# Performance work log

Measured on AMD Instinct MI355X. Metric: run time of the kernel, lower is better.

The kernel has to match this reference:

```python
import jax, jax.numpy as jnp
import numpy as np

N = 100000        # nodes
E = 1600000       # edges (avg degree 16)
F_IN = 512        # num_features
H1, D1 = 8, 8     # layer-1 heads x per-head dim (concat -> 64)
C = 16            # num_classes (layer-2: 1 head, dim C)
NEG_SLOPE = 0.2


def setup_inputs() -> dict:
    key = jax.random.key(0)
    ks = jax.random.split(key, 8)
    x = jax.random.normal(ks[0], (N, F_IN), dtype=jnp.float32)
    edge_index = jax.random.randint(ks[1], (2, E), 0, N, dtype=jnp.int64)
    W1 = jax.random.normal(ks[2], (F_IN, H1 * D1), dtype=jnp.float32) / np.float32(np.sqrt(F_IN))
    a1_src = jax.random.normal(ks[3], (H1, D1), dtype=jnp.float32) * 0.1
    a1_dst = jax.random.normal(ks[4], (H1, D1), dtype=jnp.float32) * 0.1
    W2 = jax.random.normal(ks[5], (H1 * D1, C), dtype=jnp.float32) / np.float32(np.sqrt(H1 * D1))
    a2_src = jax.random.normal(ks[6], (1, C), dtype=jnp.float32) * 0.1
    a2_dst = jax.random.normal(ks[7], (1, C), dtype=jnp.float32) * 0.1
    return {"x": x, "edge_index": edge_index, "W1": W1, "a1_src": a1_src,
            "a1_dst": a1_dst, "W2": W2, "a2_src": a2_src, "a2_dst": a2_dst}


def gat_layer(x, src, dst, W, a_s, a_d, heads, out_dim):
    """Multi-head GAT conv: gather -> per-edge leaky-relu score -> segment
    softmax over destination -> scatter-aggregate. Returns [N, heads, out_dim]."""
    n = x.shape[0]
    h = (x @ W).reshape(n, heads, out_dim)            # [N, H, D]
    es = jnp.einsum('nhd,hd->nh', h, a_s)             # source attention term
    ed = jnp.einsum('nhd,hd->nh', h, a_d)             # dest attention term
    e = jax.nn.leaky_relu(es[src] + ed[dst], NEG_SLOPE)   # [E, H]
    m = jax.ops.segment_max(e, dst, num_segments=n)       # stable softmax max
    ex = jnp.exp(e - m[dst])
    s = jax.ops.segment_sum(ex, dst, num_segments=n)
    alpha = ex / s[dst]                               # [E, H]
    out = jax.ops.segment_sum(h[src] * alpha[..., None], dst, num_segments=n)
    return out                                        # [N, H, D]


def reference(x, edge_index, W1, a1_src, a1_dst, W2, a2_src, a2_dst):
    n = x.shape[0]
    loop = jnp.arange(n, dtype=edge_index.dtype)
    src = jnp.concatenate([edge_index[0], loop])      # add self-loops
    dst = jnp.concatenate([edge_index[1], loop])
    # eval mode: dropout(p=0.6, training=False) is identity
    h1 = gat_layer(x, src, dst, W1, a1_src, a1_dst, H1, D1).reshape(n, H1 * D1)
    h1 = jax.nn.elu(h1)
    h2 = gat_layer(h1, src, dst, W2, a2_src, a2_dst, 1, C).reshape(n, C)
    return jax.nn.log_softmax(h2, axis=1)
```

## Files before the change

### kernel.cpp

```cpp
#include <hip/hip_runtime.h>
#include <hip/hip_bf16.h>

#define F_IN 512
#define H1 8
#define D1 8
#define F_MID 64
#define C 16
#define NEG_SLOPE 0.2f
#define BIN_CHUNK 4096
#define NB_MAX 1024
#define BUCKET_SHIFT 7
#define BUCKET_STRIDE 3072

typedef __attribute__((ext_vector_type(8))) short bf16x8;
typedef __attribute__((ext_vector_type(4))) float f32x4;

static __device__ __forceinline__ unsigned short f2bf(float f) {
    __hip_bfloat16 h = __float2bfloat16(f);
    return *(unsigned short*)&h;
}

__global__ __launch_bounds__(256) void k_bin(const int* __restrict__ src,
                                             const int* __restrict__ dst,
                                             int* __restrict__ gcur,
                                             int2* __restrict__ bucketed,
                                             int n_edges, int nb) {
    __shared__ int cnt[NB_MAX];
    __shared__ int base[NB_MAX];
    const int t = threadIdx.x;
    const int eb = blockIdx.x * BIN_CHUNK;
    for (int b = t; b < nb; b += 256) cnt[b] = 0;
    __syncthreads();
#pragma unroll
    for (int i = 0; i < BIN_CHUNK / 256; ++i) {
        int e = eb + i * 256 + t;
        if (e < n_edges) atomicAdd(&cnt[dst[e] >> BUCKET_SHIFT], 1);
    }
    __syncthreads();
    for (int b = t; b < nb; b += 256) {
        int c = cnt[b];
        base[b] = c > 0 ? atomicAdd(&gcur[b], c) : 0;
        cnt[b] = 0;
    }
    __syncthreads();
#pragma unroll
    for (int i = 0; i < BIN_CHUNK / 256; ++i) {
        int e = eb + i * 256 + t;
        if (e < n_edges) {
            int d = dst[e];
            int b = d >> BUCKET_SHIFT;
            int local = atomicAdd(&cnt[b], 1);
            bucketed[(size_t)b * BUCKET_STRIDE + base[b] + local] = make_int2(src[e], d);
        }
    }
}

__global__ __launch_bounds__(1024) void k_bscan(const int* __restrict__ gcur,
                                                int* __restrict__ bucket_base,
                                                int* __restrict__ row_start_last,
                                                int nb, int n_edges_total) {
    __shared__ int sh[1024];
    const int t = threadIdx.x;
    const int v = (t < nb) ? gcur[t] : 0;
    sh[t] = v;
    __syncthreads();
#pragma unroll
    for (int d = 1; d < 1024; d <<= 1) {
        int u = (t >= d) ? sh[t - d] : 0;
        __syncthreads();
        sh[t] += u;
        __syncthreads();
    }
    if (t < nb) bucket_base[t] = sh[t] - v;
    if (t == 0) *row_start_last = n_edges_total;
}

__global__ __launch_bounds__(256) void k_place(const int* __restrict__ gcur,
                                               const int* __restrict__ bucket_base,
                                               const int2* __restrict__ bucketed,
                                               int* __restrict__ row_start,
                                               int* __restrict__ sorted_src, int n_nodes) {
    __shared__ int2 stage[BUCKET_STRIDE];
    __shared__ int cnt[1 << BUCKET_SHIFT];
    __shared__ int cur[1 << BUCKET_SHIFT];
    const int t = threadIdx.x;
    const int b = blockIdx.x;
    if (t < (1 << BUCKET_SHIFT)) cnt[t] = 0;
    __syncthreads();
    const int total = gcur[b];
    const int2* bp = bucketed + (size_t)b * BUCKET_STRIDE;
    for (int i = t; i < total; i += 256) {
        int2 e = bp[i];
        stage[i] = e;
        atomicAdd(&cnt[e.y & ((1 << BUCKET_SHIFT) - 1)], 1);
    }
    __syncthreads();
    if (t < (1 << BUCKET_SHIFT)) cur[t] = cnt[t];
    __syncthreads();
#pragma unroll
    for (int d = 1; d < (1 << BUCKET_SHIFT); d <<= 1) {
        int u = 0;
        if (t < (1 << BUCKET_SHIFT) && t >= d) u = cur[t - d];
        __syncthreads();
        if (t < (1 << BUCKET_SHIFT)) cur[t] += u;
        __syncthreads();
    }
    const int base0 = bucket_base[b];
    if (t < (1 << BUCKET_SHIFT)) {
        int node = (b << BUCKET_SHIFT) + t;
        int excl = cur[t] - cnt[t];
        if (node < n_nodes) row_start[node] = base0 + excl;
        cur[t] = excl;
    }
    __syncthreads();
    for (int i = t; i < total; i += 256) {
        int2 e = stage[i];
        int p = atomicAdd(&cur[e.y & ((1 << BUCKET_SHIFT) - 1)], 1);
        sorted_src[base0 + p] = e.x;
    }
}

__global__ __launch_bounds__(256) void k_w1t(const float* __restrict__ W1,
                                             __hip_bfloat16* __restrict__ w1t) {
    int idx = blockIdx.x * 256 + threadIdx.x;
    int k = idx >> 6, n = idx & 63;
    w1t[n * F_IN + k] = __float2bfloat16(W1[idx]);
}

__global__ __launch_bounds__(256) void k_gemm1(const float* __restrict__ x,
                                               const __hip_bfloat16* __restrict__ w1t,
                                               const float* __restrict__ a1s,
                                               const float* __restrict__ a1d,
                                               __hip_bfloat16* __restrict__ h1b,
                                               float* __restrict__ es1,
                                               float* __restrict__ ed1, int n_nodes) {
    __shared__ unsigned short Xs[64][72];
    __shared__ unsigned short Ws[64][72];
    __shared__ float sas[64], sad[64];
    const int t = threadIdx.x;
    if (t < 64) sas[t] = a1s[t];
    else if (t < 128) sad[t - 64] = a1d[t - 64];

    const int wv = t >> 6, l = t & 63;
    const int q = l >> 4, m16 = l & 15;
    const int rowbase = blockIdx.x * 64;

    const int sr = t >> 2, sf = t & 3;
    int gx = rowbase + sr;
    gx = gx < n_nodes ? gx : n_nodes - 1;
    const float* xrow = x + (size_t)gx * F_IN;
    const __hip_bfloat16* wrow = w1t + (size_t)sr * F_IN;

    f32x4 acc[4];
#pragma unroll
    for (int i = 0; i < 4; ++i) acc[i] = (f32x4){0.f, 0.f, 0.f, 0.f};

    for (int kt = 0; kt < F_IN; kt += 64) {
#pragma unroll
        for (int j = 0; j < 4; ++j) {
            float4 v = *(const float4*)(xrow + kt + sf * 16 + j * 4);
            ushort4 b;
            b.x = f2bf(v.x); b.y = f2bf(v.y); b.z = f2bf(v.z); b.w = f2bf(v.w);
            *(ushort4*)&Xs[sr][sf * 16 + j * 4] = b;
        }
#pragma unroll
        for (int j = 0; j < 2; ++j) {
            *(int4*)&Ws[sr][sf * 16 + j * 8] =
                *(const int4*)(wrow + kt + sf * 16 + j * 8);
        }
        __syncthreads();
#pragma unroll
        for (int kk = 0; kk < 2; ++kk) {
            bf16x8 bfrag = *(const bf16x8*)&Xs[wv * 16 + m16][kk * 32 + q * 8];
#pragma unroll
            for (int tn = 0; tn < 4; ++tn) {
                bf16x8 afrag = *(const bf16x8*)&Ws[tn * 16 + m16][kk * 32 + q * 8];
                acc[tn] = __builtin_amdgcn_mfma_f32_16x16x32_bf16(afrag, bfrag, acc[tn], 0, 0, 0);
            }
        }
        __syncthreads();
    }

    const int node = rowbase + wv * 16 + m16;
    const bool ok = node < n_nodes;
#pragma unroll
    for (int tn = 0; tn < 4; ++tn) {
        const f32x4 a = acc[tn];
        const int nw0 = tn * 16 + q * 4;
        float vs = a.x * sas[nw0] + a.y * sas[nw0 + 1] + a.z * sas[nw0 + 2] + a.w * sas[nw0 + 3];
        float vd = a.x * sad[nw0] + a.y * sad[nw0 + 1] + a.z * sad[nw0 + 2] + a.w * sad[nw0 + 3];
        vs += __shfl_xor(vs, 16, 64);
        vd += __shfl_xor(vd, 16, 64);
        if (ok) {
            ushort4 b;
            b.x = f2bf(a.x); b.y = f2bf(a.y); b.z = f2bf(a.z); b.w = f2bf(a.w);
            *(ushort4*)(h1b + (size_t)node * F_MID + nw0) = b;
            if ((q & 1) == 0) {
                const int head = 2 * tn + (q >> 1);
                es1[node * H1 + head] = vs;
                ed1[node * H1 + head] = vd;
            }
        }
    }
}

__global__ __launch_bounds__(256) void k_gather1(const int* __restrict__ row_start,
                                                 const int* __restrict__ sorted_src,
                                                 const __hip_bfloat16* __restrict__ h1b,
                                                 const float* __restrict__ es1,
                                                 const float* __restrict__ ed1,
                                                 float* __restrict__ h1, int n_nodes) {
    const int n = blockIdx.x * 4 + (threadIdx.x >> 6);
    if (n >= n_nodes) return;
    const int lane = threadIdx.x & 63;
    const int h = lane >> 3;
    const float edh = ed1[n * H1 + h];
    const int beg = row_start[n], end = row_start[n + 1];
    float acc = 0.f, den = 0.f;
    for (int base = beg; base < end; base += 64) {
        const int m = min(64, end - base);
        const int li = lane < m ? lane : (m - 1);
        const int myS = sorted_src[base + li];
        int j = 0;
        for (; j + 4 <= m; j += 4) {
            const int s0 = __shfl(myS, j, 64), s1 = __shfl(myS, j + 1, 64);
            const int s2 = __shfl(myS, j + 2, 64), s3 = __shfl(myS, j + 3, 64);
            float e0 = es1[s0 * H1 + h], e1 = es1[s1 * H1 + h];
            float e2 = es1[s2 * H1 + h], e3 = es1[s3 * H1 + h];
            const float f0 = __bfloat162float(h1b[(size_t)s0 * F_MID + lane]);
            const float f1 = __bfloat162float(h1b[(size_t)s1 * F_MID + lane]);
            const float f2 = __bfloat162float(h1b[(size_t)s2 * F_MID + lane]);
            const float f3 = __bfloat162float(h1b[(size_t)s3 * F_MID + lane]);
            e0 += edh; e1 += edh; e2 += edh; e3 += edh;
            e0 = e0 > 0.f ? e0 : NEG_SLOPE * e0;
            e1 = e1 > 0.f ? e1 : NEG_SLOPE * e1;
            e2 = e2 > 0.f ? e2 : NEG_SLOPE * e2;
            e3 = e3 > 0.f ? e3 : NEG_SLOPE * e3;
            const float w0 = __expf(e0), w1 = __expf(e1), w2 = __expf(e2), w3 = __expf(e3);
            acc += w0 * f0 + w1 * f1 + w2 * f2 + w3 * f3;
            den += (w0 + w1) + (w2 + w3);
        }
        for (; j < m; ++j) {
            const int s = __shfl(myS, j, 64);
            float ev = es1[s * H1 + h] + edh;
            ev = ev > 0.f ? ev : NEG_SLOPE * ev;
            const float w = __expf(ev);
            acc += w * __bfloat162float(h1b[(size_t)s * F_MID + lane]);
            den += w;
        }
    }
    float evs = es1[n * H1 + h] + edh;
    evs = evs > 0.f ? evs : NEG_SLOPE * evs;
    const float ws = __expf(evs);
    acc += ws * __bfloat162float(h1b[(size_t)n * F_MID + lane]);
    den += ws;
    float v = acc / den;
    v = v > 0.f ? v : expm1f(v);
    h1[(size_t)n * F_MID + lane] = v;
}

__global__ void k_gemm2(const float* __restrict__ h1, const float* __restrict__ W2,
                        const float* __restrict__ a2s, const float* __restrict__ a2d,
                        __hip_bfloat16* __restrict__ h2b, float* __restrict__ es2,
                        float* __restrict__ ed2, int n_nodes) {
    __shared__ float w2s[F_MID * C];
    __shared__ float h1s[16][F_MID + 1];
    const int t = threadIdx.x;
    const int nb = blockIdx.x * 16;
    for (int i = t; i < F_MID * C; i += 256) w2s[i] = W2[i];
    for (int i = t; i < 16 * F_MID; i += 256) {
        int r = i >> 6, k = i & 63;
        int n = nb + r;
        h1s[r][k] = h1[(size_t)(n < n_nodes ? n : n_nodes - 1) * F_MID + k];
    }
    __syncthreads();
    const int r = t >> 4, c = t & 15;
    const int n = nb + r;
    float acc = 0.f;
#pragma unroll
    for (int k = 0; k < F_MID; ++k) acc += h1s[r][k] * w2s[k * C + c];
    float vs = acc * a2s[c], vd = acc * a2d[c];
#pragma unroll
    for (int off = 1; off < 16; off <<= 1) {
        vs += __shfl_xor(vs, off, 64);
        vd += __shfl_xor(vd, off, 64);
    }
    if (n < n_nodes) {
        h2b[(size_t)n * C + c] = __float2bfloat16(acc);
        if (c == 0) { es2[n] = vs; ed2[n] = vd; }
    }
}

__global__ __launch_bounds__(256) void k_gather2(const int* __restrict__ row_start,
                                                 const int* __restrict__ sorted_src,
                                                 const __hip_bfloat16* __restrict__ h2b,
                                                 const float* __restrict__ es2,
                                                 const float* __restrict__ ed2,
                                                 float* __restrict__ out, int n_nodes) {
    const int n = blockIdx.x * 16 + (threadIdx.x >> 4);
    if (n >= n_nodes) return;
    const int lane = threadIdx.x & 63;
    const int c = lane & 15;
    const int g = lane >> 4;
    const float ed = ed2[n];
    const int beg = row_start[n], end = row_start[n + 1];
    float acc = 0.f, den = 0.f;
    for (int base = beg; base < end; base += 16) {
        const int m = min(16, end - base);
        const int li = c < m ? c : (m - 1);
        const int myS = sorted_src[base + li];
        int j = 0;
        for (; j + 4 <= m; j += 4) {
            const int s0 = __shfl(myS, g * 16 + j, 64), s1 = __shfl(myS, g * 16 + j + 1, 64);
            const int s2 = __shfl(myS, g * 16 + j + 2, 64), s3 = __shfl(myS, g * 16 + j + 3, 64);
            float e0 = es2[s0] + ed, e1 = es2[s1] + ed, e2 = es2[s2] + ed, e3 = es2[s3] + ed;
            const float f0 = __bfloat162float(h2b[(size_t)s0 * C + c]);
            const float f1 = __bfloat162float(h2b[(size_t)s1 * C + c]);
            const float f2 = __bfloat162float(h2b[(size_t)s2 * C + c]);
            const float f3 = __bfloat162float(h2b[(size_t)s3 * C + c]);
            e0 = e0 > 0.f ? e0 : NEG_SLOPE * e0;
            e1 = e1 > 0.f ? e1 : NEG_SLOPE * e1;
            e2 = e2 > 0.f ? e2 : NEG_SLOPE * e2;
            e3 = e3 > 0.f ? e3 : NEG_SLOPE * e3;
            const float w0 = __expf(e0), w1 = __expf(e1), w2 = __expf(e2), w3 = __expf(e3);
            acc += w0 * f0 + w1 * f1 + w2 * f2 + w3 * f3;
            den += (w0 + w1) + (w2 + w3);
        }
        for (; j < m; ++j) {
            const int s = __shfl(myS, g * 16 + j, 64);
            float ev = es2[s] + ed;
            ev = ev > 0.f ? ev : NEG_SLOPE * ev;
            const float w = __expf(ev);
            acc += w * __bfloat162float(h2b[(size_t)s * C + c]);
            den += w;
        }
    }
    float evs = es2[n] + ed;
    evs = evs > 0.f ? evs : NEG_SLOPE * evs;
    const float ws = __expf(evs);
    acc += ws * __bfloat162float(h2b[(size_t)n * C + c]);
    den += ws;
    const float v = acc / den;
    float mx = v;
#pragma unroll
    for (int off = 1; off < 16; off <<= 1) mx = fmaxf(mx, __shfl_xor(mx, off, 64));
    float se = __expf(v - mx);
#pragma unroll
    for (int off = 1; off < 16; off <<= 1) se += __shfl_xor(se, off, 64);
    out[(size_t)n * C + c] = v - mx - __logf(se);
}

extern "C" void kernel_launch(void* const* d_in, const int* in_sizes, int n_in,
                              void* d_out, int out_size, void* d_ws, size_t ws_size,
                              hipStream_t stream) {
    const float* x   = (const float*)d_in[0];
    const int*   ei  = (const int*)d_in[1];
    const float* W1  = (const float*)d_in[2];
    const float* a1s = (const float*)d_in[3];
    const float* a1d = (const float*)d_in[4];
    const float* W2  = (const float*)d_in[5];
    const float* a2s = (const float*)d_in[6];
    const float* a2d = (const float*)d_in[7];
    float* out = (float*)d_out;

    const int n_nodes = in_sizes[0] / F_IN;
    const int n_edges = in_sizes[1] / 2;
    const int* src = ei;
    const int* dst = ei + n_edges;
    const int nb = (n_nodes + (1 << BUCKET_SHIFT) - 1) >> BUCKET_SHIFT;

    float* fws = (float*)d_ws;
    float* es1 = fws;
    float* ed1 = es1 + (size_t)n_nodes * H1;
    float* h1  = ed1 + (size_t)n_nodes * H1;
    float* es2 = h1  + (size_t)n_nodes * F_MID;
    float* ed2 = es2 + n_nodes;
    __hip_bfloat16* h1b = (__hip_bfloat16*)(ed2 + n_nodes);
    __hip_bfloat16* h2b = h1b + (size_t)n_nodes * F_MID;
    __hip_bfloat16* w1t = h2b + (size_t)n_nodes * C;
    int* iws         = (int*)(w1t + F_IN * F_MID);
    int* gcur        = iws;
    int* bucket_base = gcur + NB_MAX;
    int* row_start   = bucket_base + NB_MAX;
    int* sorted_src  = row_start + n_nodes + 1;
    int2* bucketed   = (int2*)(((uintptr_t)(sorted_src + n_edges) + 15) & ~(uintptr_t)15);

    hipMemsetAsync(gcur, 0, NB_MAX * sizeof(int), stream);

    k_bin<<<(n_edges + BIN_CHUNK - 1) / BIN_CHUNK, 256, 0, stream>>>(src, dst, gcur, bucketed, n_edges, nb);
    k_bscan<<<1, 1024, 0, stream>>>(gcur, bucket_base, &row_start[n_nodes], nb, n_edges);
    k_place<<<nb, 256, 0, stream>>>(gcur, bucket_base, bucketed, row_start, sorted_src, n_nodes);

    k_w1t<<<(F_IN * F_MID) / 256, 256, 0, stream>>>(W1, w1t);
    k_gemm1<<<(n_nodes + 63) / 64, 256, 0, stream>>>(x, w1t, a1s, a1d, h1b, es1, ed1, n_nodes);
    k_gather1<<<(n_nodes + 3) / 4, 256, 0, stream>>>(row_start, sorted_src, h1b, es1, ed1, h1, n_nodes);

    k_gemm2<<<(n_nodes + 15) / 16, 256, 0, stream>>>(h1, W2, a2s, a2d, h2b, es2, ed2, n_nodes);
    k_gather2<<<(n_nodes + 15) / 16, 256, 0, stream>>>(row_start, sorted_src, h2b, es2, ed2, out, n_nodes);
}
```

Baseline: 487.6 us.

## Fuse layer-2 projection into gather1 and fold bucket scan into place kernel

The layer-2 linear projection and its attention terms now run inside the layer-1 aggregation kernel. Each wave multiplies its ELU output by W2 held in shared memory and reduces across lanes with shuffles and a small LDS transpose. This drops the fp32 h1 intermediate write and read and one kernel launch. The separate single-block bucket scan is also removed: each k_place block sums the preceding bucket counts itself. The cost is redundant prefix reads per block and extra shuffle and LDS work per node in gather1.

Result: slower. 505.7 us (+3.7%).

```diff
diff --git a/kernel.cpp b/kernel.cpp
--- a/kernel.cpp
+++ b/kernel.cpp
@@ -55,38 +55,27 @@
     }
 }
 
-__global__ __launch_bounds__(1024) void k_bscan(const int* __restrict__ gcur,
-                                                int* __restrict__ bucket_base,
-                                                int* __restrict__ row_start_last,
-                                                int nb, int n_edges_total) {
-    __shared__ int sh[1024];
-    const int t = threadIdx.x;
-    const int v = (t < nb) ? gcur[t] : 0;
-    sh[t] = v;
-    __syncthreads();
-#pragma unroll
-    for (int d = 1; d < 1024; d <<= 1) {
-        int u = (t >= d) ? sh[t - d] : 0;
-        __syncthreads();
-        sh[t] += u;
-        __syncthreads();
-    }
-    if (t < nb) bucket_base[t] = sh[t] - v;
-    if (t == 0) *row_start_last = n_edges_total;
-}
-
 __global__ __launch_bounds__(256) void k_place(const int* __restrict__ gcur,
-                                               const int* __restrict__ bucket_base,
                                                const int2* __restrict__ bucketed,
                                                int* __restrict__ row_start,
-                                               int* __restrict__ sorted_src, int n_nodes) {
+                                               int* __restrict__ sorted_src,
+                                               int n_nodes, int n_edges) {
     __shared__ int2 stage[BUCKET_STRIDE];
     __shared__ int cnt[1 << BUCKET_SHIFT];
     __shared__ int cur[1 << BUCKET_SHIFT];
+    __shared__ int wsum[4];
     const int t = threadIdx.x;
     const int b = blockIdx.x;
     if (t < (1 << BUCKET_SHIFT)) cnt[t] = 0;
-    __syncthreads();
+    int pre = 0;
+    for (int j = t; j < b; j += 256) pre += gcur[j];
+#pragma unroll
+    for (int off = 1; off < 64; off <<= 1) pre += __shfl_xor(pre, off, 64);
+    if ((t & 63) == 0) wsum[t >> 6] = pre;
+    __syncthreads();
+    const int base0 = wsum[0] + wsum[1] + wsum[2] + wsum[3];
+    if (b == 0 && t == 0) row_start[n_nodes] = n_edges;
+
     const int total = gcur[b];
     const int2* bp = bucketed + (size_t)b * BUCKET_STRIDE;
     for (int i = t; i < total; i += 256) {
@@ -105,7 +94,6 @@
         if (t < (1 << BUCKET_SHIFT)) cur[t] += u;
         __syncthreads();
     }
-    const int base0 = bucket_base[b];
     if (t < (1 << BUCKET_SHIFT)) {
         int node = (b << BUCKET_SHIFT) + t;
         int excl = cur[t] - cnt[t];
@@ -209,10 +197,33 @@
                                                  const __hip_bfloat16* __restrict__ h1b,
                                                  const float* __restrict__ es1,
                                                  const float* __restrict__ ed1,
-                                                 float* __restrict__ h1, int n_nodes) {
-    const int n = blockIdx.x * 4 + (threadIdx.x >> 6);
+                                                 const float* __restrict__ W2,
+                                                 const float* __restrict__ a2s,
+                                                 const float* __restrict__ a2d,
+                                                 __hip_bfloat16* __restrict__ h2b,
+                                                 float* __restrict__ es2,
+                                                 float* __restrict__ ed2, int n_nodes) {
+    __shared__ float w2t[16 * 64];
+    __shared__ float tbuf[4][16 * 17];
+    __shared__ float sa2s[16], sa2d[16];
+    const int t = threadIdx.x;
+    {
+        const int i = t * 4;
+#pragma unroll
+        for (int j = 0; j < 4; ++j) {
+            int idx = i + j;
+            w2t[(idx & 15) * 64 + (idx >> 4)] = W2[idx];
+        }
+        if (t < 16) sa2s[t] = a2s[t];
+        else if (t < 32) sa2d[t - 16] = a2d[t - 16];
+    }
+    __syncthreads();
+
+    const int n = blockIdx.x * 4 + (t >> 6);
+    const int lane = t & 63;
+    const int wv = t >> 6;
     if (n >= n_nodes) return;
-    const int lane = threadIdx.x & 63;
+
     const int h = lane >> 3;
     const float edh = ed1[n * H1 + h];
     const int beg = row_start[n], end = row_start[n + 1];
@@ -256,39 +267,30 @@
     den += ws;
     float v = acc / den;
     v = v > 0.f ? v : expm1f(v);
-    h1[(size_t)n * F_MID + lane] = v;
-}
-
-__global__ void k_gemm2(const float* __restrict__ h1, const float* __restrict__ W2,
-                        const float* __restrict__ a2s, const float* __restrict__ a2d,
-                        __hip_bfloat16* __restrict__ h2b, float* __restrict__ es2,
-                        float* __restrict__ ed2, int n_nodes) {
-    __shared__ float w2s[F_MID * C];
-    __shared__ float h1s[16][F_MID + 1];
-    const int t = threadIdx.x;
-    const int nb = blockIdx.x * 16;
-    for (int i = t; i < F_MID * C; i += 256) w2s[i] = W2[i];
-    for (int i = t; i < 16 * F_MID; i += 256) {
-        int r = i >> 6, k = i & 63;
-        int n = nb + r;
-        h1s[r][k] = h1[(size_t)(n < n_nodes ? n : n_nodes - 1) * F_MID + k];
-    }
-    __syncthreads();
-    const int r = t >> 4, c = t & 15;
-    const int n = nb + r;
-    float acc = 0.f;
-#pragma unroll
-    for (int k = 0; k < F_MID; ++k) acc += h1s[r][k] * w2s[k * C + c];
-    float vs = acc * a2s[c], vd = acc * a2d[c];
+
+    float p[16];
+#pragma unroll
+    for (int c = 0; c < 16; ++c) p[c] = v * w2t[c * 64 + lane];
+#pragma unroll
+    for (int c = 0; c < 16; ++c) p[c] += __shfl_xor(p[c], 16, 64);
+#pragma unroll
+    for (int c = 0; c < 16; ++c) p[c] += __shfl_xor(p[c], 32, 64);
+    const int m16 = lane & 15;
+    const int jg = lane >> 4;
+    float* tw = tbuf[wv];
+#pragma unroll
+    for (int j = 0; j < 4; ++j) tw[(jg * 4 + j) * 17 + m16] = p[jg * 4 + j];
+    float S = 0.f;
+#pragma unroll
+    for (int mm = 0; mm < 16; ++mm) S += tw[m16 * 17 + mm];
+    float vs = S * sa2s[m16], vd = S * sa2d[m16];
 #pragma unroll
     for (int off = 1; off < 16; off <<= 1) {
         vs += __shfl_xor(vs, off, 64);
         vd += __shfl_xor(vd, off, 64);
     }
-    if (n < n_nodes) {
-        h2b[(size_t)n * C + c] = __float2bfloat16(acc);
-        if (c == 0) { es2[n] = vs; ed2[n] = vd; }
-    }
+    if (lane < 16) h2b[(size_t)n * C + m16] = __float2bfloat16(S);
+    if (lane == 0) { es2[n] = vs; ed2[n] = vd; }
 }
 
 __global__ __launch_bounds__(256) void k_gather2(const int* __restrict__ row_start,
@@ -372,29 +374,26 @@
     float* fws = (float*)d_ws;
     float* es1 = fws;
     float* ed1 = es1 + (size_t)n_nodes * H1;
-    float* h1  = ed1 + (size_t)n_nodes * H1;
-    float* es2 = h1  + (size_t)n_nodes * F_MID;
+    float* es2 = ed1 + (size_t)n_nodes * H1;
     float* ed2 = es2 + n_nodes;
     __hip_bfloat16* h1b = (__hip_bfloat16*)(ed2 + n_nodes);
     __hip_bfloat16* h2b = h1b + (size_t)n_nodes * F_MID;
     __hip_bfloat16* w1t = h2b + (size_t)n_nodes * C;
     int* iws         = (int*)(w1t + F_IN * F_MID);
     int* gcur        = iws;
-    int* bucket_base = gcur + NB_MAX;
-    int* row_start   = bucket_base + NB_MAX;
+    int* row_start   = gcur + NB_MAX;
     int* sorted_src  = row_start + n_nodes + 1;
     int2* bucketed   = (int2*)(((uintptr_t)(sorted_src + n_edges) + 15) & ~(uintptr_t)15);
 
     hipMemsetAsync(gcur, 0, NB_MAX * sizeof(int), stream);
 
     k_bin<<<(n_edges + BIN_CHUNK - 1) / BIN_CHUNK, 256, 0, stream>>>(src, dst, gcur, bucketed, n_edges, nb);
-    k_bscan<<<1, 1024, 0, stream>>>(gcur, bucket_base, &row_start[n_nodes], nb, n_edges);
-    k_place<<<nb, 256, 0, stream>>>(gcur, bucket_base, bucketed, row_start, sorted_src, n_nodes);
+    k_place<<<nb, 256, 0, stream>>>(gcur, bucketed, row_start, sorted_src, n_nodes, n_edges);
 
     k_w1t<<<(F_IN * F_MID) / 256, 256, 0, stream>>>(W1, w1t);
     k_gemm1<<<(n_nodes + 63) / 64, 256, 0, stream>>>(x, w1t, a1s, a1d, h1b, es1, ed1, n_nodes);
-    k_gather1<<<(n_nodes + 3) / 4, 256, 0, stream>>>(row_start, sorted_src, h1b, es1, ed1, h1, n_nodes);
-
-    k_gemm2<<<(n_nodes + 15) / 16, 256, 0, stream>>>(h1, W2, a2s, a2d, h2b, es2, ed2, n_nodes);
+    k_gather1<<<(n_nodes + 3) / 4, 256, 0, stream>>>(row_start, sorted_src, h1b, es1, ed1,
+                                                     W2, a2s, a2d, h2b, es2, ed2, n_nodes);
+
     k_gather2<<<(n_nodes + 15) / 16, 256, 0, stream>>>(row_start, sorted_src, h2b, es2, ed2, out, n_nodes);
 }
```

## Pack bucketed edges into one int and fold bucket scan into placement

Applied to the files above, without the earlier changes.

Each bucketed edge is now stored as one 32-bit word, with the low 7 bits of the destination packed above a 17-bit source index, instead of an int2. This halves the scatter traffic in binning and the reads in placement, and halves the LDS staging buffer. The separate single-block bucket scan kernel is removed; each placement block instead sums the counts of all earlier buckets itself with a wave reduction, saving one launch. The packing assumes node ids fit in 17 bits, which holds for N=100000, and each block now redoes a redundant prefix sum over up to about 800 counts.

Result: no change. 482.1 us (-1.1%).

```diff
diff --git a/kernel.cpp b/kernel.cpp
--- a/kernel.cpp
+++ b/kernel.cpp
@@ -11,6 +11,8 @@
 #define NB_MAX 1024
 #define BUCKET_SHIFT 7
 #define BUCKET_STRIDE 3072
+#define SRC_BITS 17
+#define SRC_MASK ((1 << SRC_BITS) - 1)
 
 typedef __attribute__((ext_vector_type(8))) short bf16x8;
 typedef __attribute__((ext_vector_type(4))) float f32x4;
@@ -23,7 +25,7 @@
 __global__ __launch_bounds__(256) void k_bin(const int* __restrict__ src,
                                              const int* __restrict__ dst,
                                              int* __restrict__ gcur,
-                                             int2* __restrict__ bucketed,
+                                             int* __restrict__ bucketed,
                                              int n_edges, int nb) {
     __shared__ int cnt[NB_MAX];
     __shared__ int base[NB_MAX];
@@ -50,49 +52,39 @@
             int d = dst[e];
             int b = d >> BUCKET_SHIFT;
             int local = atomicAdd(&cnt[b], 1);
-            bucketed[(size_t)b * BUCKET_STRIDE + base[b] + local] = make_int2(src[e], d);
-        }
-    }
-}
-
-__global__ __launch_bounds__(1024) void k_bscan(const int* __restrict__ gcur,
-                                                int* __restrict__ bucket_base,
-                                                int* __restrict__ row_start_last,
-                                                int nb, int n_edges_total) {
-    __shared__ int sh[1024];
-    const int t = threadIdx.x;
-    const int v = (t < nb) ? gcur[t] : 0;
-    sh[t] = v;
-    __syncthreads();
-#pragma unroll
-    for (int d = 1; d < 1024; d <<= 1) {
-        int u = (t >= d) ? sh[t - d] : 0;
-        __syncthreads();
-        sh[t] += u;
-        __syncthreads();
-    }
-    if (t < nb) bucket_base[t] = sh[t] - v;
-    if (t == 0) *row_start_last = n_edges_total;
+            bucketed[(size_t)b * BUCKET_STRIDE + base[b] + local] =
+                ((d & ((1 << BUCKET_SHIFT) - 1)) << SRC_BITS) | src[e];
+        }
+    }
 }
 
 __global__ __launch_bounds__(256) void k_place(const int* __restrict__ gcur,
-                                               const int* __restrict__ bucket_base,
-                                               const int2* __restrict__ bucketed,
+                                               const int* __restrict__ bucketed,
                                                int* __restrict__ row_start,
-                                               int* __restrict__ sorted_src, int n_nodes) {
-    __shared__ int2 stage[BUCKET_STRIDE];
+                                               int* __restrict__ sorted_src,
+                                               int n_nodes, int n_edges) {
+    __shared__ int stage[BUCKET_STRIDE];
     __shared__ int cnt[1 << BUCKET_SHIFT];
     __shared__ int cur[1 << BUCKET_SHIFT];
+    __shared__ int wsum[4];
     const int t = threadIdx.x;
     const int b = blockIdx.x;
     if (t < (1 << BUCKET_SHIFT)) cnt[t] = 0;
-    __syncthreads();
+    int pre = 0;
+    for (int j = t; j < b; j += 256) pre += gcur[j];
+#pragma unroll
+    for (int off = 1; off < 64; off <<= 1) pre += __shfl_xor(pre, off, 64);
+    if ((t & 63) == 0) wsum[t >> 6] = pre;
+    __syncthreads();
+    const int base0 = wsum[0] + wsum[1] + wsum[2] + wsum[3];
+    if (b == 0 && t == 0) row_start[n_nodes] = n_edges;
+
     const int total = gcur[b];
-    const int2* bp = bucketed + (size_t)b * BUCKET_STRIDE;
+    const int* bp = bucketed + (size_t)b * BUCKET_STRIDE;
     for (int i = t; i < total; i += 256) {
-        int2 e = bp[i];
+        int e = bp[i];
         stage[i] = e;
-        atomicAdd(&cnt[e.y & ((1 << BUCKET_SHIFT) - 1)], 1);
+        atomicAdd(&cnt[e >> SRC_BITS], 1);
     }
     __syncthreads();
     if (t < (1 << BUCKET_SHIFT)) cur[t] = cnt[t];
@@ -105,7 +97,6 @@
         if (t < (1 << BUCKET_SHIFT)) cur[t] += u;
         __syncthreads();
     }
-    const int base0 = bucket_base[b];
     if (t < (1 << BUCKET_SHIFT)) {
         int node = (b << BUCKET_SHIFT) + t;
         int excl = cur[t] - cnt[t];
@@ -114,9 +105,9 @@
     }
     __syncthreads();
     for (int i = t; i < total; i += 256) {
-        int2 e = stage[i];
-        int p = atomicAdd(&cur[e.y & ((1 << BUCKET_SHIFT) - 1)], 1);
-        sorted_src[base0 + p] = e.x;
+        int e = stage[i];
+        int p = atomicAdd(&cur[e >> SRC_BITS], 1);
+        sorted_src[base0 + p] = e & SRC_MASK;
     }
 }
 
@@ -380,16 +371,14 @@
     __hip_bfloat16* w1t = h2b + (size_t)n_nodes * C;
     int* iws         = (int*)(w1t + F_IN * F_MID);
     int* gcur        = iws;
-    int* bucket_base = gcur + NB_MAX;
-    int* row_start   = bucket_base + NB_MAX;
+    int* row_start   = gcur + NB_MAX;
     int* sorted_src  = row_start + n_nodes + 1;
-    int2* bucketed   = (int2*)(((uintptr_t)(sorted_src + n_edges) + 15) & ~(uintptr_t)15);
+    int* bucketed    = sorted_src + n_edges;
 
     hipMemsetAsync(gcur, 0, NB_MAX * sizeof(int), stream);
 
     k_bin<<<(n_edges + BIN_CHUNK - 1) / BIN_CHUNK, 256, 0, stream>>>(src, dst, gcur, bucketed, n_edges, nb);
-    k_bscan<<<1, 1024, 0, stream>>>(gcur, bucket_base, &row_start[n_nodes], nb, n_edges);
-    k_place<<<nb, 256, 0, stream>>>(gcur, bucket_base, bucketed, row_start, sorted_src, n_nodes);
+    k_place<<<nb, 256, 0, stream>>>(gcur, bucketed, row_start, sorted_src, n_nodes, n_edges);
 
     k_w1t<<<(F_IN * F_MID) / 256, 256, 0, stream>>>(W1, w1t);
     k_gemm1<<<(n_nodes + 63) / 64, 256, 0, stream>>>(x, w1t, a1s, a1d, h1b, es1, ed1, n_nodes);
```
